# Performance work log

Measured on AMD Instinct MI355X. Metric: run time of the kernel, lower is better.

## Reference

```python
import jax, jax.numpy as jnp
import numpy as np

B, T, D = 256, 512, 128


def setup_inputs() -> dict:
    key = jax.random.key(0)
    ks = jax.random.split(key, 10)
    s = 0.05
    return {
        "x": jax.random.normal(ks[0], (B, T, D), jnp.float32),
        "lengths": jax.random.randint(ks[1], (B,), 1, T + 1, dtype=jnp.int32),
        "Wa": jax.random.normal(ks[2], (D, 3 * D), jnp.float32) * s,
        "Ua": jax.random.normal(ks[3], (D, 3 * D), jnp.float32) * s,
        "ba_in": jnp.zeros((3 * D,), jnp.float32),
        "ba_rec": jnp.zeros((3 * D,), jnp.float32),
        "Wb": jax.random.normal(ks[4], (D, 3 * D), jnp.float32) * s,
        "Ub": jax.random.normal(ks[5], (D, 3 * D), jnp.float32) * s,
        "bb_in": jnp.zeros((3 * D,), jnp.float32),
        "bb_rec": jnp.zeros((3 * D,), jnp.float32),
        "W_alpha": jax.random.normal(ks[6], (D, 1), jnp.float32) * s,
        "b_alpha": jnp.zeros((1,), jnp.float32),
        "W_beta": jax.random.normal(ks[7], (D, D), jnp.float32) * s,
        "b_beta": jnp.zeros((D,), jnp.float32),
    }


def _masked_gru(xp, mask_t, U, b_rec):
    # Keras GRU v2 (reset_after=True). xp: [T,B,3D] input projections (+input bias),
    # mask_t: [T,B]. Masked steps carry state forward (Keras mask semantics).
    h0 = jnp.zeros((xp.shape[1], U.shape[0]), xp.dtype)

    def step(h, inp):
        xt, mt = inp
        rp = h @ U + b_rec                      # [B,3D] recurrent projection
        xz, xr, xh = jnp.split(xt, 3, axis=-1)
        rz, rr, rh = jnp.split(rp, 3, axis=-1)
        z = jax.nn.sigmoid(xz + rz)
        r = jax.nn.sigmoid(xr + rr)
        hh = jnp.tanh(xh + r * rh)
        hn = z * h + (1.0 - z) * hh
        hn = jnp.where(mt[:, None], hn, h)
        return hn, hn

    _, hs = jax.lax.scan(step, h0, (xp, mask_t))
    return hs  # [T,B,D]


def _forward(x, lengths, Wa, Ua, ba_in, ba_rec, Wb, Ub, bb_in, bb_rec,
             W_alpha, b_alpha, W_beta, b_beta):
    Tn = x.shape[1]
    t = jnp.arange(Tn)
    valid = t[None, :] < lengths[:, None]                      # [B,T]
    # vectorized per-sample reverse of the first `length` steps, zeros after
    ridx = jnp.clip(lengths[:, None] - 1 - t[None, :], 0, Tn - 1)
    rx = jnp.take_along_axis(x, ridx[:, :, None], axis=1)
    rx = jnp.where(valid[:, :, None], rx, jnp.zeros((), x.dtype))

    mask_t = valid.T                                            # [T,B]
    g = _masked_gru(jnp.einsum('btd,de->tbe', rx, Wa) + ba_in, mask_t, Ua, ba_rec)
    h = _masked_gru(jnp.einsum('btd,de->tbe', rx, Wb) + bb_in, mask_t, Ub, bb_rec)
    g = jnp.transpose(g, (1, 0, 2))                             # [B,T,D]
    h = jnp.transpose(h, (1, 0, 2))

    attn_alpha = jax.nn.softmax(g @ W_alpha + b_alpha, axis=1)  # [B,T,1] over time
    attn_beta = jnp.tanh(h @ W_beta + b_beta)                   # [B,T,D]
    return jnp.sum(attn_alpha * attn_beta * x, axis=1)          # [B,D]


def reference(x, lengths, Wa, Ua, ba_in, ba_rec, Wb, Ub, bb_in, bb_rec,
              W_alpha, b_alpha, W_beta, b_beta):
    return _forward(x, lengths, Wa, Ua, ba_in, ba_rec, Wb, Ub, bb_in, bb_rec,
                    W_alpha, b_alpha, W_beta, b_beta)
```

## Files before the change

kernel.cpp:

```cpp
#include <hip/hip_runtime.h>
#include <hip/hip_bf16.h>
#include <math.h>


#define BATCH 256
#define TLEN  512
#define DDIM  128
#define G3    384

static const size_t HB_SZ = (size_t)BATCH * TLEN * DDIM;
static const size_t E_SZ  = (size_t)BATCH * TLEN;

__device__ __forceinline__ int clamp_len(int l) {
    return l < 1 ? 1 : (l > TLEN ? TLEN : l);
}

__device__ __forceinline__ float sigm_f(float s) {
    s = fminf(fmaxf(s, -30.f), 30.f);
    return __fdividef(1.f, 1.f + __expf(-s));
}
__device__ __forceinline__ float tanh_f(float u) {
    u = fminf(fmaxf(u, -15.f), 15.f);
    const float e2 = __expf(2.f * u);
    return __fdividef(e2 - 1.f, e2 + 1.f);
}

template<bool BF16>
__device__ __forceinline__ float loadH(const void* p, size_t i) {
    if constexpr (BF16) return __bfloat162float(((const __hip_bfloat16*)p)[i]);
    else return ((const float*)p)[i];
}

template<bool STORE_BF16>
__global__ __launch_bounds__(512, 2) void retain_gru_persist(
    const float* __restrict__ x, const int* __restrict__ lengths,
    const float* __restrict__ Wa, const float* __restrict__ Ua,
    const float* __restrict__ ba_in, const float* __restrict__ ba_rec,
    const float* __restrict__ Wb, const float* __restrict__ Ub,
    const float* __restrict__ bb_in, const float* __restrict__ bb_rec,
    const float* __restrict__ W_alpha, const float* __restrict__ b_alpha,
    void* __restrict__ hBv, float* __restrict__ e)
{
    const int g  = blockIdx.x & 1;
    const int ip = blockIdx.x >> 1;

    const int tid  = threadIdx.x;
    const int isU  = tid >= 256;
    const int tt   = tid & 255;
    const int half = tt >> 7;
    const int c    = tt & 127;

    __shared__ int lensh[BATCH];
    __shared__ int rank2b[BATCH];
    __shared__ __align__(16) float xsh[2][DDIM];
    __shared__ __align__(16) float hsh[DDIM];
    __shared__ float partX[2][G3];
    __shared__ float partU[2][G3];
    __shared__ float sred[2];

    if (tid < BATCH) lensh[tid] = clamp_len(lengths[tid]);
    __syncthreads();
    if (tid < BATCH) {
        const int myl = lensh[tid];
        int rank = 0;
        for (int j = 0; j < BATCH; ++j) {
            const int lj = lensh[j];
            rank += (lj > myl) || (lj == myl && j < tid);
        }
        rank2b[rank] = tid;
    }

    const float* __restrict__ M = isU ? (g ? Ub : Ua) : (g ? Wb : Wa);
    float Wr0[64], Wr1[64], Wr2[64];
    #pragma unroll
    for (int r = 0; r < 64; ++r) {
        const float* row = M + (size_t)(half * 64 + r) * G3 + c;
        Wr0[r] = row[0]; Wr1[r] = row[128]; Wr2[r] = row[256];
    }
    const float* __restrict__ bias = isU ? (g ? bb_rec : ba_rec) : (g ? bb_in : ba_in);
    const float i0 = half ? 0.f : bias[c];
    const float i1 = half ? 0.f : bias[c + 128];
    const float i2 = half ? 0.f : bias[c + 256];

    float wal = 0.f, balv = 0.f;
    if (tid < DDIM) { wal = W_alpha[tid]; balv = b_alpha[0]; }
    __syncthreads();

    for (int jj = 0; jj < 2; ++jj) {
        const int b   = rank2b[jj == 0 ? ip : (255 - ip)];
        const int len = lensh[b];

        if (tid < DDIM) {
            hsh[tid] = 0.f;
            xsh[0][tid] = x[((size_t)b * TLEN + (len - 1)) * DDIM + tid];
        }
        __syncthreads();

        for (int t = 0; t < len; ++t) {
            float xnext = 0.f;
            if (tid < DDIM) {
                int rn = len - 2 - t; if (rn < 0) rn = 0;
                xnext = x[((size_t)b * TLEN + rn) * DDIM + tid];
            }

            const float* __restrict__ vh =
                (isU ? hsh : xsh[t & 1]) + half * 64;
            float a0 = i0, a1 = i1, a2 = i2;
            float c0 = 0.f, c1 = 0.f, c2 = 0.f;
            #pragma unroll
            for (int rr = 0; rr < 32; rr += 4) {
                const float4 v = *reinterpret_cast<const float4*>(vh + rr);
                a0 = fmaf(v.x, Wr0[rr+0], a0); a1 = fmaf(v.x, Wr1[rr+0], a1); a2 = fmaf(v.x, Wr2[rr+0], a2);
                a0 = fmaf(v.y, Wr0[rr+1], a0); a1 = fmaf(v.y, Wr1[rr+1], a1); a2 = fmaf(v.y, Wr2[rr+1], a2);
                a0 = fmaf(v.z, Wr0[rr+2], a0); a1 = fmaf(v.z, Wr1[rr+2], a1); a2 = fmaf(v.z, Wr2[rr+2], a2);
                a0 = fmaf(v.w, Wr0[rr+3], a0); a1 = fmaf(v.w, Wr1[rr+3], a1); a2 = fmaf(v.w, Wr2[rr+3], a2);
            }
            #pragma unroll
            for (int rr = 32; rr < 64; rr += 4) {
                const float4 v = *reinterpret_cast<const float4*>(vh + rr);
                c0 = fmaf(v.x, Wr0[rr+0], c0); c1 = fmaf(v.x, Wr1[rr+0], c1); c2 = fmaf(v.x, Wr2[rr+0], c2);
                c0 = fmaf(v.y, Wr0[rr+1], c0); c1 = fmaf(v.y, Wr1[rr+1], c1); c2 = fmaf(v.y, Wr2[rr+1], c2);
                c0 = fmaf(v.z, Wr0[rr+2], c0); c1 = fmaf(v.z, Wr1[rr+2], c1); c2 = fmaf(v.z, Wr2[rr+2], c2);
                c0 = fmaf(v.w, Wr0[rr+3], c0); c1 = fmaf(v.w, Wr1[rr+3], c1); c2 = fmaf(v.w, Wr2[rr+3], c2);
            }
            float* __restrict__ P = isU ? partU[half] : partX[half];
            P[c] = a0 + c0; P[c + 128] = a1 + c1; P[c + 256] = a2 + c2;
            __syncthreads();

            if (tid < DDIM) {
                const int d = tid;
                const float xz = partX[0][d]       + partX[1][d];
                const float xr = partX[0][128 + d] + partX[1][128 + d];
                const float xh = partX[0][256 + d] + partX[1][256 + d];
                const float rz  = partU[0][d]       + partU[1][d];
                const float rr_ = partU[0][128 + d] + partU[1][128 + d];
                const float rh  = partU[0][256 + d] + partU[1][256 + d];
                const float z  = sigm_f(xz + rz);
                const float rg = sigm_f(xr + rr_);
                const float hh = tanh_f(xh + rg * rh);
                const float hn = z * hsh[d] + (1.f - z) * hh;
                hsh[d] = hn;
                xsh[(t & 1) ^ 1][d] = xnext;
                if (g) {
                    const size_t oi = ((size_t)b * TLEN + t) * DDIM + d;
                    if constexpr (STORE_BF16) ((__hip_bfloat16*)hBv)[oi] = __float2bfloat16(hn);
                    else                      ((float*)hBv)[oi] = hn;
                } else {
                    float pa = hn * wal;
                    #pragma unroll
                    for (int off = 32; off > 0; off >>= 1) pa += __shfl_down(pa, off);
                    if ((tid & 63) == 0) sred[tid >> 6] = pa;
                }
            }
            __syncthreads();
            if (!g && tid == 0) e[(size_t)b * TLEN + t] = sred[0] + sred[1] + balv;
        }
        __syncthreads();
    }
}

template<bool HB_BF16>
__global__ __launch_bounds__(256) void retain_attn(
    const float* __restrict__ x, const int* __restrict__ lengths,
    const float* __restrict__ W_beta, const float* __restrict__ b_beta,
    const void* __restrict__ hBv, const float* __restrict__ eb,
    float* __restrict__ out)
{
    const int bid   = blockIdx.x;
    const int b     = bid >> 1;
    const int thalf = bid & 1;
    const int len   = clamp_len(lengths[b]);
    const float* __restrict__ e = eb + (size_t)b * TLEN;

    const int tid = threadIdx.x;
    const int d   = tid & 127;
    const int rh  = tid >> 7;

    float Wreg[64];
    #pragma unroll
    for (int rr = 0; rr < 64; rr++) Wreg[rr] = W_beta[(rh * 64 + rr) * DDIM + d];
    const float bb = b_beta[d];

    __shared__ float se[512];
    __shared__ float red[256];
    __shared__ __align__(16) float h2[2][128];
    __shared__ float part[2][2][128];

    for (int idx = tid; idx < 512; idx += 256) {
        const int tc = idx < len ? idx : len - 1;
        se[idx] = e[tc];
    }
    __syncthreads();
    red[tid] = fmaxf(se[tid], se[tid + 256]);
    __syncthreads();
    for (int s = 128; s > 0; s >>= 1) {
        if (tid < s) red[tid] = fmaxf(red[tid], red[tid + s]);
        __syncthreads();
    }
    const float mx = red[0];
    __syncthreads();
    const float s0 = expf(se[tid] - mx), s1 = expf(se[tid + 256] - mx);
    se[tid] = s0; se[tid + 256] = s1;
    red[tid] = s0 + s1;
    __syncthreads();
    for (int s = 128; s > 0; s >>= 1) {
        if (tid < s) red[tid] += red[tid + s];
        __syncthreads();
    }
    const float inv = 1.f / red[0];
    __syncthreads();

    const int tbase = thalf * 256;
    float acc = 0.f;
    for (int tp = 0; tp < 256; tp += 2) {
        const int t0 = tbase + tp;
        {
            const int t  = t0 + rh;
            const int tc = t < len ? t : len - 1;
            h2[rh][d] = loadH<HB_BF16>(hBv, ((size_t)b * TLEN + tc) * DDIM + d);
        }
        __syncthreads();
        float p0 = 0.f, p1 = 0.f;
        #pragma unroll
        for (int rr = 0; rr < 64; rr += 4) {
            const float4 ha = *reinterpret_cast<const float4*>(&h2[0][rh * 64 + rr]);
            const float4 hb = *reinterpret_cast<const float4*>(&h2[1][rh * 64 + rr]);
            p0 = fmaf(ha.x, Wreg[rr + 0], p0);
            p0 = fmaf(ha.y, Wreg[rr + 1], p0);
            p0 = fmaf(ha.z, Wreg[rr + 2], p0);
            p0 = fmaf(ha.w, Wreg[rr + 3], p0);
            p1 = fmaf(hb.x, Wreg[rr + 0], p1);
            p1 = fmaf(hb.y, Wreg[rr + 1], p1);
            p1 = fmaf(hb.z, Wreg[rr + 2], p1);
            p1 = fmaf(hb.w, Wreg[rr + 3], p1);
        }
        part[rh][0][d] = p0;
        part[rh][1][d] = p1;
        __syncthreads();
        if (rh == 0) {
            #pragma unroll
            for (int ti = 0; ti < 2; ti++) {
                const int t = t0 + ti;
                const float v  = tanhf(part[0][ti][d] + part[1][ti][d] + bb);
                const float al = se[t] * inv;
                const float xv = x[((size_t)b * TLEN + t) * DDIM + d];
                acc = fmaf(al * v, xv, acc);
            }
        }
        __syncthreads();
    }
    if (rh == 0) atomicAdd(&out[b * DDIM + d], acc);
}

extern "C" void kernel_launch(void* const* d_in, const int* in_sizes, int n_in,
                              void* d_out, int out_size, void* d_ws, size_t ws_size,
                              hipStream_t stream)
{
    const float* x       = (const float*)d_in[0];
    const int*   lengths = (const int*)  d_in[1];
    const float* Wa      = (const float*)d_in[2];
    const float* Ua      = (const float*)d_in[3];
    const float* ba_in   = (const float*)d_in[4];
    const float* ba_rec  = (const float*)d_in[5];
    const float* Wb      = (const float*)d_in[6];
    const float* Ub      = (const float*)d_in[7];
    const float* bb_in   = (const float*)d_in[8];
    const float* bb_rec  = (const float*)d_in[9];
    const float* W_alpha = (const float*)d_in[10];
    const float* b_alpha = (const float*)d_in[11];
    const float* W_beta  = (const float*)d_in[12];
    const float* b_beta  = (const float*)d_in[13];
    float* out = (float*)d_out;
    float* ws  = (float*)d_ws;

    const size_t need_f32  = (HB_SZ + E_SZ) * sizeof(float);
    const size_t need_bf16 = HB_SZ * 2 + E_SZ * sizeof(float);

    hipMemsetAsync(d_out, 0, (size_t)out_size * sizeof(float), stream);

    if (ws_size >= need_f32) {
        float* hB = ws;
        float* e  = ws + HB_SZ;
        retain_gru_persist<false><<<256, 512, 0, stream>>>(
            x, lengths, Wa, Ua, ba_in, ba_rec, Wb, Ub, bb_in, bb_rec, W_alpha, b_alpha, hB, e);
        retain_attn<false><<<512, 256, 0, stream>>>(x, lengths, W_beta, b_beta, hB, e, out);
    } else if (ws_size >= need_bf16) {
        void*  hB = (void*)ws;
        float* e  = (float*)((char*)d_ws + HB_SZ * 2);
        retain_gru_persist<true><<<256, 512, 0, stream>>>(
            x, lengths, Wa, Ua, ba_in, ba_rec, Wb, Ub, bb_in, bb_rec, W_alpha, b_alpha, hB, e);
        retain_attn<true><<<512, 256, 0, stream>>>(x, lengths, W_beta, b_beta, hB, e, out);
    }
}
```

Baseline: 1.032 ms.

## Rework GRU recurrence with 768 threads, double-buffered state and deferred alpha logits

Result: slower. 1.090 ms (+5.6%).

```diff
diff --git a/kernel.cpp b/kernel.cpp
--- a/kernel.cpp
+++ b/kernel.cpp
@@ -1,5 +1,5 @@
 #include <hip/hip_runtime.h>
-#include <hip/hip_bf16.h>
+#include <hip/hip_fp16.h>
 #include <math.h>
 
 
@@ -14,7 +14,6 @@
 __device__ __forceinline__ int clamp_len(int l) {
     return l < 1 ? 1 : (l > TLEN ? TLEN : l);
 }
-
 __device__ __forceinline__ float sigm_f(float s) {
     s = fminf(fmaxf(s, -30.f), 30.f);
     return __fdividef(1.f, 1.f + __expf(-s));
@@ -25,40 +24,33 @@
     return __fdividef(e2 - 1.f, e2 + 1.f);
 }
 
-template<bool BF16>
-__device__ __forceinline__ float loadH(const void* p, size_t i) {
-    if constexpr (BF16) return __bfloat162float(((const __hip_bfloat16*)p)[i]);
-    else return ((const float*)p)[i];
-}
-
-template<bool STORE_BF16>
-__global__ __launch_bounds__(512, 2) void retain_gru_persist(
+__global__ __launch_bounds__(768, 3) void retain_gru_v3(
     const float* __restrict__ x, const int* __restrict__ lengths,
     const float* __restrict__ Wa, const float* __restrict__ Ua,
     const float* __restrict__ ba_in, const float* __restrict__ ba_rec,
     const float* __restrict__ Wb, const float* __restrict__ Ub,
     const float* __restrict__ bb_in, const float* __restrict__ bb_rec,
     const float* __restrict__ W_alpha, const float* __restrict__ b_alpha,
-    void* __restrict__ hBv, float* __restrict__ e)
+    __half* __restrict__ hB, float* __restrict__ e)
 {
-    const int g  = blockIdx.x & 1;
-    const int ip = blockIdx.x >> 1;
-
-    const int tid  = threadIdx.x;
-    const int isU  = tid >= 256;
-    const int tt   = tid & 255;
-    const int half = tt >> 7;
-    const int c    = tt & 127;
+    const int g   = blockIdx.x & 1;
+    const int ip  = blockIdx.x >> 1;
+    const int tid = threadIdx.x;
+    const int m   = (tid >= 384) ? 1 : 0;
+    const int tp  = tid - 384 * m;
+    const int q   = tp / 96;
+    const int c4  = (tp - q * 96) * 4;
 
     __shared__ int lensh[BATCH];
     __shared__ int rank2b[BATCH];
     __shared__ __align__(16) float xsh[2][DDIM];
-    __shared__ __align__(16) float hsh[DDIM];
-    __shared__ float partX[2][G3];
-    __shared__ float partU[2][G3];
-    __shared__ float sred[2];
+    __shared__ __align__(16) float hsh[2][DDIM];
+    __shared__ __align__(16) float parts[2][4][G3];
+    __shared__ __align__(16) float walsh[DDIM];
+    __shared__ __align__(16) float ep8[2][8];
 
     if (tid < BATCH) lensh[tid] = clamp_len(lengths[tid]);
+    if (tid < DDIM)  walsh[tid] = W_alpha[tid];
     __syncthreads();
     if (tid < BATCH) {
         const int myl = lensh[tid];
@@ -70,28 +62,29 @@
         rank2b[rank] = tid;
     }
 
-    const float* __restrict__ M = isU ? (g ? Ub : Ua) : (g ? Wb : Wa);
-    float Wr0[64], Wr1[64], Wr2[64];
+    const float* __restrict__ Mw = m ? (g ? Ub : Ua) : (g ? Wb : Wa);
+    float W0[32], W1[32], W2[32], W3[32];
     #pragma unroll
-    for (int r = 0; r < 64; ++r) {
-        const float* row = M + (size_t)(half * 64 + r) * G3 + c;
-        Wr0[r] = row[0]; Wr1[r] = row[128]; Wr2[r] = row[256];
-    }
-    const float* __restrict__ bias = isU ? (g ? bb_rec : ba_rec) : (g ? bb_in : ba_in);
-    const float i0 = half ? 0.f : bias[c];
-    const float i1 = half ? 0.f : bias[c + 128];
-    const float i2 = half ? 0.f : bias[c + 256];
-
-    float wal = 0.f, balv = 0.f;
-    if (tid < DDIM) { wal = W_alpha[tid]; balv = b_alpha[0]; }
+    for (int r = 0; r < 32; ++r) {
+        const float4 wv = *reinterpret_cast<const float4*>(Mw + (size_t)(q * 32 + r) * G3 + c4);
+        W0[r] = wv.x; W1[r] = wv.y; W2[r] = wv.z; W3[r] = wv.w;
+    }
+
+    float bi0 = 0, bi1 = 0, bi2 = 0, br0 = 0, br1 = 0, br2 = 0, balv = 0;
+    if (tid < DDIM) {
+        const float* bi = g ? bb_in  : ba_in;
+        const float* br = g ? bb_rec : ba_rec;
+        bi0 = bi[tid]; bi1 = bi[tid + 128]; bi2 = bi[tid + 256];
+        br0 = br[tid]; br1 = br[tid + 128]; br2 = br[tid + 256];
+    }
+    if (tid == 136) balv = b_alpha[0];
     __syncthreads();
 
     for (int jj = 0; jj < 2; ++jj) {
-        const int b   = rank2b[jj == 0 ? ip : (255 - ip)];
+        const int b   = rank2b[jj ? 255 - ip : ip];
         const int len = lensh[b];
-
         if (tid < DDIM) {
-            hsh[tid] = 0.f;
+            hsh[1][tid] = 0.f;
             xsh[0][tid] = x[((size_t)b * TLEN + (len - 1)) * DDIM + tid];
         }
         __syncthreads();
@@ -102,74 +95,100 @@
                 int rn = len - 2 - t; if (rn < 0) rn = 0;
                 xnext = x[((size_t)b * TLEN + rn) * DDIM + tid];
             }
-
-            const float* __restrict__ vh =
-                (isU ? hsh : xsh[t & 1]) + half * 64;
-            float a0 = i0, a1 = i1, a2 = i2;
-            float c0 = 0.f, c1 = 0.f, c2 = 0.f;
+            const float* __restrict__ vh = (m ? hsh[(t + 1) & 1] : xsh[t & 1]) + q * 32;
+            float A0 = 0.f, A1 = 0.f, A2 = 0.f, A3 = 0.f;
             #pragma unroll
             for (int rr = 0; rr < 32; rr += 4) {
                 const float4 v = *reinterpret_cast<const float4*>(vh + rr);
-                a0 = fmaf(v.x, Wr0[rr+0], a0); a1 = fmaf(v.x, Wr1[rr+0], a1); a2 = fmaf(v.x, Wr2[rr+0], a2);
-                a0 = fmaf(v.y, Wr0[rr+1], a0); a1 = fmaf(v.y, Wr1[rr+1], a1); a2 = fmaf(v.y, Wr2[rr+1], a2);
-                a0 = fmaf(v.z, Wr0[rr+2], a0); a1 = fmaf(v.z, Wr1[rr+2], a1); a2 = fmaf(v.z, Wr2[rr+2], a2);
-                a0 = fmaf(v.w, Wr0[rr+3], a0); a1 = fmaf(v.w, Wr1[rr+3], a1); a2 = fmaf(v.w, Wr2[rr+3], a2);
-            }
-            #pragma unroll
-            for (int rr = 32; rr < 64; rr += 4) {
-                const float4 v = *reinterpret_cast<const float4*>(vh + rr);
-                c0 = fmaf(v.x, Wr0[rr+0], c0); c1 = fmaf(v.x, Wr1[rr+0], c1); c2 = fmaf(v.x, Wr2[rr+0], c2);
-                c0 = fmaf(v.y, Wr0[rr+1], c0); c1 = fmaf(v.y, Wr1[rr+1], c1); c2 = fmaf(v.y, Wr2[rr+1], c2);
-                c0 = fmaf(v.z, Wr0[rr+2], c0); c1 = fmaf(v.z, Wr1[rr+2], c1); c2 = fmaf(v.z, Wr2[rr+2], c2);
-                c0 = fmaf(v.w, Wr0[rr+3], c0); c1 = fmaf(v.w, Wr1[rr+3], c1); c2 = fmaf(v.w, Wr2[rr+3], c2);
-            }
-            float* __restrict__ P = isU ? partU[half] : partX[half];
-            P[c] = a0 + c0; P[c + 128] = a1 + c1; P[c + 256] = a2 + c2;
+                A0 = fmaf(v.x, W0[rr+0], A0); A1 = fmaf(v.x, W1[rr+0], A1);
+                A2 = fmaf(v.x, W2[rr+0], A2); A3 = fmaf(v.x, W3[rr+0], A3);
+                A0 = fmaf(v.y, W0[rr+1], A0); A1 = fmaf(v.y, W1[rr+1], A1);
+                A2 = fmaf(v.y, W2[rr+1], A2); A3 = fmaf(v.y, W3[rr+1], A3);
+                A0 = fmaf(v.z, W0[rr+2], A0); A1 = fmaf(v.z, W1[rr+2], A1);
+                A2 = fmaf(v.z, W2[rr+2], A2); A3 = fmaf(v.z, W3[rr+2], A3);
+                A0 = fmaf(v.w, W0[rr+3], A0); A1 = fmaf(v.w, W1[rr+3], A1);
+                A2 = fmaf(v.w, W2[rr+3], A2); A3 = fmaf(v.w, W3[rr+3], A3);
+            }
+            *reinterpret_cast<float4*>(&parts[m][q][c4]) = float4{A0, A1, A2, A3};
             __syncthreads();
 
             if (tid < DDIM) {
                 const int d = tid;
-                const float xz = partX[0][d]       + partX[1][d];
-                const float xr = partX[0][128 + d] + partX[1][128 + d];
-                const float xh = partX[0][256 + d] + partX[1][256 + d];
-                const float rz  = partU[0][d]       + partU[1][d];
-                const float rr_ = partU[0][128 + d] + partU[1][128 + d];
-                const float rh  = partU[0][256 + d] + partU[1][256 + d];
+                const float xz = bi0 + parts[0][0][d]     + parts[0][1][d]     + parts[0][2][d]     + parts[0][3][d];
+                const float xr = bi1 + parts[0][0][128+d] + parts[0][1][128+d] + parts[0][2][128+d] + parts[0][3][128+d];
+                const float xh = bi2 + parts[0][0][256+d] + parts[0][1][256+d] + parts[0][2][256+d] + parts[0][3][256+d];
+                const float rz = br0 + parts[1][0][d]     + parts[1][1][d]     + parts[1][2][d]     + parts[1][3][d];
+                const float rr_= br1 + parts[1][0][128+d] + parts[1][1][128+d] + parts[1][2][128+d] + parts[1][3][128+d];
+                const float rh = br2 + parts[1][0][256+d] + parts[1][1][256+d] + parts[1][2][256+d] + parts[1][3][256+d];
                 const float z  = sigm_f(xz + rz);
-                const float rg = sigm_f(xr + rr_);
-                const float hh = tanh_f(xh + rg * rh);
-                const float hn = z * hsh[d] + (1.f - z) * hh;
-                hsh[d] = hn;
-                xsh[(t & 1) ^ 1][d] = xnext;
-                if (g) {
-                    const size_t oi = ((size_t)b * TLEN + t) * DDIM + d;
-                    if constexpr (STORE_BF16) ((__hip_bfloat16*)hBv)[oi] = __float2bfloat16(hn);
-                    else                      ((float*)hBv)[oi] = hn;
-                } else {
-                    float pa = hn * wal;
+                const float r_ = sigm_f(xr + rr_);
+                const float hh = tanh_f(xh + r_ * rh);
+                const float hn = z * hsh[(t + 1) & 1][d] + (1.f - z) * hh;
+                hsh[t & 1][d] = hn;
+                xsh[(t + 1) & 1][d] = xnext;
+                if (g) hB[((size_t)b * TLEN + t) * DDIM + d] = __float2half(hn);
+            } else if (!g && tid >= 128 && tid < 136) {
+                if (t >= 1) {
+                    const int k0 = (tid - 128) * 16;
+                    const float* hp = hsh[(t + 1) & 1];
+                    float s = 0.f;
                     #pragma unroll
-                    for (int off = 32; off > 0; off >>= 1) pa += __shfl_down(pa, off);
-                    if ((tid & 63) == 0) sred[tid >> 6] = pa;
+                    for (int i2 = 0; i2 < 16; i2 += 4) {
+                        const float4 hv = *reinterpret_cast<const float4*>(hp + k0 + i2);
+                        const float4 wv = *reinterpret_cast<const float4*>(&walsh[k0 + i2]);
+                        s = fmaf(hv.w, wv.w, fmaf(hv.z, wv.z, fmaf(hv.y, wv.y, fmaf(hv.x, wv.x, s))));
+                    }
+                    ep8[(t + 1) & 1][tid - 128] = s;
                 }
-            }
-            __syncthreads();
-            if (!g && tid == 0) e[(size_t)b * TLEN + t] = sred[0] + sred[1] + balv;
-        }
-        __syncthreads();
-    }
-}
-
-template<bool HB_BF16>
-__global__ __launch_bounds__(256) void retain_attn(
+            } else if (!g && tid == 136 && t >= 2) {
+                float s = balv;
+                #pragma unroll
+                for (int i2 = 0; i2 < 8; ++i2) s += ep8[t & 1][i2];
+                e[(size_t)b * TLEN + (t - 2)] = s;
+            }
+            asm volatile("s_waitcnt lgkmcnt(0)" ::: "memory");
+            __builtin_amdgcn_s_barrier();
+            __builtin_amdgcn_sched_barrier(0);
+        }
+
+        if (!g && tid >= 128 && tid < 136) {
+            const int k0 = (tid - 128) * 16;
+            const float* hp = hsh[(len + 1) & 1];
+            float s = 0.f;
+            #pragma unroll
+            for (int i2 = 0; i2 < 16; i2 += 4) {
+                const float4 hv = *reinterpret_cast<const float4*>(hp + k0 + i2);
+                const float4 wv = *reinterpret_cast<const float4*>(&walsh[k0 + i2]);
+                s = fmaf(hv.w, wv.w, fmaf(hv.z, wv.z, fmaf(hv.y, wv.y, fmaf(hv.x, wv.x, s))));
+            }
+            ep8[(len + 1) & 1][tid - 128] = s;
+        } else if (!g && tid == 136 && len >= 2) {
+            float s = balv;
+            #pragma unroll
+            for (int i2 = 0; i2 < 8; ++i2) s += ep8[len & 1][i2];
+            e[(size_t)b * TLEN + (len - 2)] = s;
+        }
+        __syncthreads();
+        if (!g && tid == 136) {
+            float s = balv;
+            #pragma unroll
+            for (int i2 = 0; i2 < 8; ++i2) s += ep8[(len + 1) & 1][i2];
+            e[(size_t)b * TLEN + (len - 1)] = s;
+        }
+        __syncthreads();
+    }
+}
+
+__global__ __launch_bounds__(256, 4) void retain_attn_h(
     const float* __restrict__ x, const int* __restrict__ lengths,
     const float* __restrict__ W_beta, const float* __restrict__ b_beta,
-    const void* __restrict__ hBv, const float* __restrict__ eb,
+    const __half* __restrict__ hB, const float* __restrict__ eb,
     float* __restrict__ out)
 {
-    const int bid   = blockIdx.x;
-    const int b     = bid >> 1;
-    const int thalf = bid & 1;
-    const int len   = clamp_len(lengths[b]);
+    const int bid = blockIdx.x;
+    const int b   = bid >> 2;
+    const int tq  = bid & 3;
+    const int len = clamp_len(lengths[b]);
     const float* __restrict__ e = eb + (size_t)b * TLEN;
 
     const int tid = threadIdx.x;
@@ -210,14 +229,14 @@
     const float inv = 1.f / red[0];
     __syncthreads();
 
-    const int tbase = thalf * 256;
+    const int tbase = tq * 128;
     float acc = 0.f;
-    for (int tp = 0; tp < 256; tp += 2) {
+    for (int tp = 0; tp < 128; tp += 2) {
         const int t0 = tbase + tp;
         {
             const int t  = t0 + rh;
             const int tc = t < len ? t : len - 1;
-            h2[rh][d] = loadH<HB_BF16>(hBv, ((size_t)b * TLEN + tc) * DDIM + d);
+            h2[rh][d] = __half2float(hB[((size_t)b * TLEN + tc) * DDIM + d]);
         }
         __syncthreads();
         float p0 = 0.f, p1 = 0.f;
@@ -271,24 +290,15 @@
     const float* W_beta  = (const float*)d_in[12];
     const float* b_beta  = (const float*)d_in[13];
     float* out = (float*)d_out;
-    float* ws  = (float*)d_ws;
-
-    const size_t need_f32  = (HB_SZ + E_SZ) * sizeof(float);
-    const size_t need_bf16 = HB_SZ * 2 + E_SZ * sizeof(float);
+
+    const size_t need = HB_SZ * sizeof(__half) + E_SZ * sizeof(float);
+    if (ws_size < need) return;
+
+    __half* hB = (__half*)d_ws;
+    float*  e  = (float*)((char*)d_ws + HB_SZ * sizeof(__half));
 
     hipMemsetAsync(d_out, 0, (size_t)out_size * sizeof(float), stream);
-
-    if (ws_size >= need_f32) {
-        float* hB = ws;
-        float* e  = ws + HB_SZ;
-        retain_gru_persist<false><<<256, 512, 0, stream>>>(
-            x, lengths, Wa, Ua, ba_in, ba_rec, Wb, Ub, bb_in, bb_rec, W_alpha, b_alpha, hB, e);
-        retain_attn<false><<<512, 256, 0, stream>>>(x, lengths, W_beta, b_beta, hB, e, out);
-    } else if (ws_size >= need_bf16) {
-        void*  hB = (void*)ws;
-        float* e  = (float*)((char*)d_ws + HB_SZ * 2);
-        retain_gru_persist<true><<<256, 512, 0, stream>>>(
-            x, lengths, Wa, Ua, ba_in, ba_rec, Wb, Ub, bb_in, bb_rec, W_alpha, b_alpha, hB, e);
-        retain_attn<true><<<512, 256, 0, stream>>>(x, lengths, W_beta, b_beta, hB, e, out);
-    }
-}
+    retain_gru_v3<<<256, 768, 0, stream>>>(
+        x, lengths, Wa, Ua, ba_in, ba_rec, Wb, Ub, bb_in, bb_rec, W_alpha, b_alpha, hB, e);
+    retain_attn_h<<<1024, 256, 0, stream>>>(x, lengths, W_beta, b_beta, hB, e, out);
+}
```
